# Kernel tuning notes

Measured on AMD Instinct MI355X. Metric: run time of the kernel, lower is better.

The kernel has to match this reference:

```python
import jax, jax.numpy as jnp
import numpy as np
import math

N, S, T, E, H = 2, 2048, 2048, 1024, 16
HD = E // H  # head_dim = 64


def setup_inputs() -> dict:
    key = jax.random.key(0)
    ks = jax.random.split(key, 11)
    scale = 1.0 / math.sqrt(E)
    inp = {
        "query": jax.random.normal(ks[0], (N, S, E), jnp.float32),
        "key": jax.random.normal(ks[1], (N, T, E), jnp.float32),
        "value": jax.random.normal(ks[2], (N, T, E), jnp.float32),
        "Wq": jax.random.normal(ks[3], (E, E), jnp.float32) * scale,
        "bq": jnp.zeros((E,), jnp.float32),
        "Wk": jax.random.normal(ks[4], (E, E), jnp.float32) * scale,
        "bk": jnp.zeros((E,), jnp.float32),
        "Wv": jax.random.normal(ks[5], (E, E), jnp.float32) * scale,
        "bv": jnp.zeros((E,), jnp.float32),
        "Wo": jax.random.normal(ks[6], (E, E), jnp.float32) * scale,
        "bo": jnp.zeros((E,), jnp.float32),
    }
    return inp


def reference(query, key, value, Wq, bq, Wk, bk, Wv, bv, Wo, bo):
    # QKV projections, then split heads: [N, S, E] -> [N, H, S, HD]
    q = (query @ Wq + bq).reshape(N, S, H, HD).transpose(0, 2, 1, 3)
    k = (key @ Wk + bk).reshape(N, T, H, HD).transpose(0, 2, 1, 3)
    v = (value @ Wv + bv).reshape(N, T, H, HD).transpose(0, 2, 1, 3)
    # scaled dot-product attention scores [N, H, S, T]
    scores = jnp.einsum('nhse,nhte->nhst', q, k) / math.sqrt(HD)
    attn = jax.nn.softmax(scores, axis=-1)
    # dropout is identity in eval mode
    out = jnp.einsum('nhst,nhte->nhse', attn, v)  # [N, H, S, HD]
    out = out.transpose(0, 2, 1, 3).reshape(N, S, E)
    return out @ Wo + bo
```

## Files before the change

### kernel.cpp

```cpp
#include <hip/hip_runtime.h>
#include <hip/hip_bf16.h>

typedef __bf16 bf16x8 __attribute__((ext_vector_type(8)));
typedef __bf16 bf16x4 __attribute__((ext_vector_type(4)));
typedef float  f32x4  __attribute__((ext_vector_type(4)));
typedef float  f32x16 __attribute__((ext_vector_type(16)));
typedef unsigned int u32x4 __attribute__((ext_vector_type(4)));

#define MFMA16(a, b, c) __builtin_amdgcn_mfma_f32_16x16x32_bf16((a), (b), (c), 0, 0, 0)
#define MFMA32(a, b, c) __builtin_amdgcn_mfma_f32_32x32x16_bf16((a), (b), (c), 0, 0, 0)

constexpr int SEQ = 2048, EMB = 1024, NHEAD = 16, HD = 64;
constexpr float SSCALE = 0.18033688f;

__device__ __forceinline__ void glds16(const void* g, void* l) {
    __builtin_amdgcn_global_load_lds(
        (const __attribute__((address_space(1))) void*)g,
        (__attribute__((address_space(3))) void*)l, 16, 0, 0);
}

__global__ __launch_bounds__(256)
void prep(const float* __restrict__ W0, const float* __restrict__ W1,
          const float* __restrict__ W2, const float* __restrict__ W3,
          __bf16* __restrict__ T0, __bf16* __restrict__ T1,
          __bf16* __restrict__ T2, __bf16* __restrict__ T3,
          const float* __restrict__ X0, const float* __restrict__ X1,
          const float* __restrict__ X2, __bf16* __restrict__ Y0,
          __bf16* __restrict__ Y1, __bf16* __restrict__ Y2)
{
    __shared__ float tile[32][33];
    const int z = blockIdx.z;
    if (z < 4) {
        const float* W = (z==0) ? W0 : (z==1) ? W1 : (z==2) ? W2 : W3;
        __bf16*      T = (z==0) ? T0 : (z==1) ? T1 : (z==2) ? T2 : T3;
        const float s = (z == 0) ? SSCALE : 1.0f;
        const int kb = blockIdx.x * 32, nb = blockIdx.y * 32;
        const int c = threadIdx.x & 31, r0 = threadIdx.x >> 5;
#pragma unroll
        for (int i = 0; i < 4; ++i)
            tile[r0 + 8*i][c] = W[(size_t)(kb + r0 + 8*i)*1024 + nb + c];
        __syncthreads();
#pragma unroll
        for (int i = 0; i < 4; ++i)
            T[(size_t)(nb + r0 + 8*i)*1024 + kb + c] = (__bf16)(tile[c][r0 + 8*i] * s);
    } else {
        const float* X = (z==4) ? X0 : (z==5) ? X1 : X2;
        __bf16*      Y = (z==4) ? Y0 : (z==5) ? Y1 : Y2;
        const size_t base =
            ((size_t)(blockIdx.y * 32 + blockIdx.x) * 256 + threadIdx.x) * 16;
#pragma unroll
        for (int j = 0; j < 2; ++j) {
            const float4* s4 = (const float4*)(X + base + j*8);
            float4 f0 = s4[0], f1 = s4[1];
            bf16x8 v;
            v[0]=(__bf16)f0.x; v[1]=(__bf16)f0.y; v[2]=(__bf16)f0.z; v[3]=(__bf16)f0.w;
            v[4]=(__bf16)f1.x; v[5]=(__bf16)f1.y; v[6]=(__bf16)f1.z; v[7]=(__bf16)f1.w;
            *(bf16x8*)(Y + base + j*8) = v;
        }
    }
}

struct GArg { const __bf16* A; const __bf16* Bt; const float* bias; void* C;
              int mode; int kbase; int kcount; float bscale; };
struct GArgs3 { GArg a[3]; };

__global__ __launch_bounds__(256)
void gemmk(GArgs3 args)
{
    const int lin = blockIdx.x + (blockIdx.y << 5) + (blockIdx.z << 8);
    const int nid = (lin & 7) * 96 + (lin >> 3);
    const int gz = nid >> 8, rem = nid & 255;
    const int bm = rem >> 3, bn = rem & 7;
    const GArg g = args.a[gz];
    __shared__ __attribute__((aligned(16))) __bf16 sm[2*128*64];
    __bf16* As = sm;
    __bf16* Bs = sm + 128*64;
    const int tid = threadIdx.x, lane = tid & 63, wave = tid >> 6;
    const int wm = wave >> 1, wn = wave & 1;
    const int quad = lane >> 4, l16 = lane & 15;

    f32x4 acc[4][4] = {};

    for (int kt = 0; kt < g.kcount; ++kt) {
        const int k0 = g.kbase + kt*64;
        __syncthreads();
#pragma unroll
        for (int j = 0; j < 4; ++j) {
            const int ci = j*256 + tid;
            const int row = ci >> 3, cg = ((ci & 7) ^ (row & 7)) * 8;
            glds16(g.A + (size_t)(bm*128 + row)*1024 + k0 + cg,
                   &As[(j*256 + wave*64)*8]);
        }
#pragma unroll
        for (int j = 0; j < 4; ++j) {
            const int ci = j*256 + tid;
            const int row = ci >> 3, cg = ((ci & 7) ^ (row & 7)) * 8;
            glds16(g.Bt + (size_t)(bn*128 + row)*1024 + k0 + cg,
                   &Bs[(j*256 + wave*64)*8]);
        }
        __syncthreads();
#pragma unroll
        for (int ks = 0; ks < 2; ++ks) {
            const int kc = ks*4 + quad;
            bf16x8 af[4], bfr[4];
#pragma unroll
            for (int mt = 0; mt < 4; ++mt) {
                const int ar = wm*64 + mt*16 + l16;
                af[mt] = *(const bf16x8*)&As[ar*64 + (kc ^ (ar & 7))*8];
            }
#pragma unroll
            for (int nt = 0; nt < 4; ++nt) {
                const int br = wn*64 + nt*16 + l16;
                bfr[nt] = *(const bf16x8*)&Bs[br*64 + (kc ^ (br & 7))*8];
            }
#pragma unroll
            for (int mt = 0; mt < 4; ++mt)
#pragma unroll
                for (int nt = 0; nt < 4; ++nt)
                    acc[mt][nt] = MFMA16(af[mt], bfr[nt], acc[mt][nt]);
        }
    }

    if (g.mode == 0) {
        __syncthreads();
        __bf16* Cs = sm;
#pragma unroll
        for (int nt = 0; nt < 4; ++nt) {
            const int n = wn*64 + nt*16 + l16;
            const float bvs = g.bias[bn*128 + n] * g.bscale;
#pragma unroll
            for (int mt = 0; mt < 4; ++mt) {
                const int mb = wm*64 + mt*16 + quad*4;
                f32x4 v = acc[mt][nt];
#pragma unroll
                for (int r = 0; r < 4; ++r) {
                    const int m = mb + r;
                    Cs[m*128 + (((n >> 3) ^ (m & 7)) * 8) + (n & 7)] =
                        (__bf16)(v[r] + bvs);
                }
            }
        }
        __syncthreads();
        __bf16* C = (__bf16*)g.C;
        const int p8 = tid & 7;
#pragma unroll
        for (int ps = 0; ps < 8; ++ps) {
            const int run = ps * 32 + (tid >> 3);
            const int m = run >> 1, hh = run & 1;
            const int gm = bm*128 + m;
            const int nb = gm >> 11, s = gm & 2047;
            const int h = bn*2 + hh;
            bf16x8 val = *(const bf16x8*)&Cs[m*128 + (((hh*8 + p8) ^ (m & 7)) * 8)];
            *(bf16x8*)&C[(size_t)(nb*NHEAD + h)*(SEQ*HD) + (size_t)s*HD + p8*8] = val;
        }
    } else {
#pragma unroll
        for (int nt = 0; nt < 4; ++nt) {
            const int n = bn*128 + wn*64 + nt*16 + l16;
            const float bvs = (g.bias ? g.bias[n] : 0.f) * g.bscale;
#pragma unroll
            for (int mt = 0; mt < 4; ++mt) {
                const int mbase = bm*128 + wm*64 + mt*16 + quad*4;
                f32x4 v = acc[mt][nt];
                __bf16* C = (__bf16*)g.C;
                const int h = n >> 6, d = n & 63;
                const int nb = mbase >> 11, s = mbase & 2047;
                const int tg = (s >> 2) & 7;
                const int pg = (tg & 4) | ((tg & 1) << 1) | ((tg & 2) >> 1);
                const int sp = (s & ~31) | (pg << 2);
                bf16x4 o;
#pragma unroll
                for (int r = 0; r < 4; ++r) o[r] = (__bf16)(v[r] + bvs);
                *(bf16x4*)&C[(size_t)(nb*NHEAD + h)*(SEQ*HD) + (size_t)d*SEQ + sp] = o;
            }
        }
    }
}

__global__ __launch_bounds__(256)
void gemmo(const __bf16* __restrict__ A, const __bf16* __restrict__ Bt,
           const float* __restrict__ bias, float* __restrict__ C)
{
    const int lin = blockIdx.x + (blockIdx.y << 5);
    const int nid = (lin & 7) * 32 + (lin >> 3);
    const int bm = nid >> 3, bn = nid & 7;
    __shared__ __attribute__((aligned(16))) __bf16 As[128*64];
    __shared__ __attribute__((aligned(16))) __bf16 Bs[128*64];
    const int tid = threadIdx.x, lane = tid & 63, wave = tid >> 6;
    const int wm = wave >> 1, wn = wave & 1;
    const int quad = lane >> 4, l16 = lane & 15;

    f32x4 acc[4][4] = {};

    for (int k0 = 0; k0 < 1024; k0 += 64) {
        __syncthreads();
#pragma unroll
        for (int j = 0; j < 4; ++j) {
            const int ci = j*256 + tid;
            const int row = ci >> 3, cg = ((ci & 7) ^ (row & 7)) * 8;
            glds16(A + (size_t)(bm*128 + row)*1024 + k0 + cg,
                   &As[(j*256 + wave*64)*8]);
        }
#pragma unroll
        for (int j = 0; j < 4; ++j) {
            const int ci = j*256 + tid;
            const int row = ci >> 3, cg = ((ci & 7) ^ (row & 7)) * 8;
            glds16(Bt + (size_t)(bn*128 + row)*1024 + k0 + cg,
                   &Bs[(j*256 + wave*64)*8]);
        }
        __syncthreads();
#pragma unroll
        for (int ks = 0; ks < 2; ++ks) {
            const int kc = ks*4 + quad;
            bf16x8 af[4], bfr[4];
#pragma unroll
            for (int mt = 0; mt < 4; ++mt) {
                const int ar = wm*64 + mt*16 + l16;
                af[mt] = *(const bf16x8*)&As[ar*64 + (kc ^ (ar & 7))*8];
            }
#pragma unroll
            for (int nt = 0; nt < 4; ++nt) {
                const int br = wn*64 + nt*16 + l16;
                bfr[nt] = *(const bf16x8*)&Bs[br*64 + (kc ^ (br & 7))*8];
            }
#pragma unroll
            for (int mt = 0; mt < 4; ++mt)
#pragma unroll
                for (int nt = 0; nt < 4; ++nt)
                    acc[mt][nt] = MFMA16(af[mt], bfr[nt], acc[mt][nt]);
        }
    }
#pragma unroll
    for (int nt = 0; nt < 4; ++nt) {
        const int n = bn*128 + wn*64 + nt*16 + l16;
        const float bv = bias[n];
#pragma unroll
        for (int mt = 0; mt < 4; ++mt) {
            const int mbase = bm*128 + wm*64 + mt*16 + quad*4;
            f32x4 v = acc[mt][nt];
#pragma unroll
            for (int r = 0; r < 4; ++r)
                C[(size_t)(mbase + r)*1024 + n] = v[r] + bv;
        }
    }
}

__global__ __launch_bounds__(512, 2)
void attn32(const __bf16* __restrict__ qg, const __bf16* __restrict__ kg,
            const __bf16* __restrict__ vg, __bf16* __restrict__ Og)
{
    __shared__ __attribute__((aligned(16))) char smem[64*1024];
    float* Xch = (float*)smem;

    const int tid = threadIdx.x, lane = tid & 63, wave = tid >> 6;
    const int w4 = wave & 3, grp = wave >> 2;
    const int l32 = lane & 31, half = lane >> 5;
    const int nh = blockIdx.y;
    const int q0 = blockIdx.x * 128;
    const __bf16* qb = qg + (size_t)nh * (SEQ*HD);
    const __bf16* kb = kg + (size_t)nh * (SEQ*HD);
    const __bf16* vb = vg + (size_t)nh * (SEQ*HD);

    bf16x8 qf[4];
#pragma unroll
    for (int ks = 0; ks < 4; ++ks)
        qf[ks] = *(const bf16x8*)(qb + (size_t)(q0 + w4*32 + l32)*HD + ks*16 + half*8);

    f32x16 oacc[2] = {};
    float psum = 0.0f;

    const int cK0 = tid, rK0 = cK0 >> 3;
    const int cK1 = 512 + tid, rK1 = cK1 >> 3;
    const __bf16* kp0 = kb + (size_t)rK0*HD + ((cK0 & 7) ^ (rK0 & 7)) * 8;
    const __bf16* kp1 = kb + (size_t)rK1*HD + ((cK1 & 7) ^ (rK1 & 7)) * 8;
    const int cV0 = tid, rV0 = cV0 >> 4, pV0 = cV0 & 15;
    const int cV1 = 512 + tid, rV1 = cV1 >> 4, pV1 = cV1 & 15;
    const __bf16* vp0 = vb + (size_t)rV0*SEQ + (((pV0 & ~7) | ((pV0 & 7) ^ (rV0 & 7))) * 8);
    const __bf16* vp1 = vb + (size_t)rV1*SEQ + (((pV1 & ~7) | ((pV1 & 7) ^ (rV1 & 7))) * 8);

    auto stage = [&](int b) {
        char* Kd = smem + b * 16384;
        char* Vd = smem + 32768 + b * 16384;
        glds16(kp0, Kd + wave*1024);
        glds16(kp1, Kd + 8192 + wave*1024);
        glds16(vp0, Vd + wave*1024);
        glds16(vp1, Vd + 8192 + wave*1024);
        kp0 += 128*HD; kp1 += 128*HD;
        vp0 += 128;    vp1 += 128;
    };

    stage(0);
    int cur = 0;
    for (int it = 0; it < 16; ++it) {
        __syncthreads();
        if (it < 15) stage(cur ^ 1);

        const __bf16* Ks = (const __bf16*)(smem + cur * 16384);
        const __bf16* Vs = (const __bf16*)(smem + 32768 + cur * 16384);

        f32x16 sc[2] = {};
        __builtin_amdgcn_s_setprio(1);
#pragma unroll
        for (int ks = 0; ks < 4; ++ks) {
            const int c = ks*2 + half;
#pragma unroll
            for (int nt = 0; nt < 2; ++nt) {
                const int kr = grp*64 + nt*32 + l32;
                bf16x8 kf = *(const bf16x8*)&Ks[kr*64 + ((c ^ (kr & 7))*8)];
                sc[nt] = MFMA32(kf, qf[ks], sc[nt]);
            }
        }
        __builtin_amdgcn_s_setprio(0);

#pragma unroll
        for (int nt = 0; nt < 2; ++nt)
#pragma unroll
            for (int sub = 0; sub < 2; ++sub) {
                const float e0 = __builtin_amdgcn_exp2f(sc[nt][sub*8 + 0]);
                const float e1 = __builtin_amdgcn_exp2f(sc[nt][sub*8 + 1]);
                const float e2 = __builtin_amdgcn_exp2f(sc[nt][sub*8 + 2]);
                const float e3 = __builtin_amdgcn_exp2f(sc[nt][sub*8 + 3]);
                const float e4 = __builtin_amdgcn_exp2f(sc[nt][sub*8 + 4]);
                const float e5 = __builtin_amdgcn_exp2f(sc[nt][sub*8 + 5]);
                const float e6 = __builtin_amdgcn_exp2f(sc[nt][sub*8 + 6]);
                const float e7 = __builtin_amdgcn_exp2f(sc[nt][sub*8 + 7]);
                psum += ((e0 + e1) + (e2 + e3)) + ((e4 + e5) + (e6 + e7));
                u32x4 pk;
                asm("v_cvt_pk_bf16_f32 %0, %1, %2" : "=v"(pk.x) : "v"(e0), "v"(e1));
                asm("v_cvt_pk_bf16_f32 %0, %1, %2" : "=v"(pk.y) : "v"(e2), "v"(e3));
                asm("v_cvt_pk_bf16_f32 %0, %1, %2" : "=v"(pk.z) : "v"(e4), "v"(e5));
                asm("v_cvt_pk_bf16_f32 %0, %1, %2" : "=v"(pk.w) : "v"(e6), "v"(e7));
                const bf16x8 pf = __builtin_bit_cast(bf16x8, pk);
                const int c2 = grp*8 + (nt*2 + sub)*2 + half;
                __builtin_amdgcn_s_setprio(1);
#pragma unroll
                for (int dt = 0; dt < 2; ++dt) {
                    const int vr = dt*32 + l32;
                    const int pos = (c2 & ~7) | ((c2 & 7) ^ (vr & 7));
                    bf16x8 vf = *(const bf16x8*)&Vs[vr*128 + pos*8];
                    oacc[dt] = MFMA32(pf, vf, oacc[dt]);
                }
                __builtin_amdgcn_s_setprio(0);
            }
        cur ^= 1;
    }

    __syncthreads();
    if (grp == 1) {
        float* dst = &Xch[((w4*64) + lane) * 33];
#pragma unroll
        for (int i = 0; i < 16; ++i) {
            dst[i]      = oacc[0][i];
            dst[16 + i] = oacc[1][i];
        }
        dst[32] = psum;
    }
    __syncthreads();
    if (grp == 0) {
        const float* src = &Xch[((w4*64) + lane) * 33];
#pragma unroll
        for (int i = 0; i < 16; ++i) {
            oacc[0][i] += src[i];
            oacc[1][i] += src[16 + i];
        }
        psum += src[32];
        psum += __shfl(psum, lane ^ 32);
        float* dl = (float*)(smem + 60*1024);
        if (half == 0) dl[w4*32 + l32] = psum;
        const int nb = nh >> 4, h = nh & 15;
#pragma unroll
        for (int reg = 0; reg < 16; ++reg) {
            const int row = (reg & 3) + 8*(reg >> 2) + 4*half;
            const int srow = q0 + w4*32 + row;
            const float inv = 1.0f / dl[w4*32 + row];
#pragma unroll
            for (int dt = 0; dt < 2; ++dt)
                Og[(size_t)(nb*SEQ + srow)*EMB + h*HD + dt*32 + l32] =
                    (__bf16)(oacc[dt][reg] * inv);
        }
    }
}

extern "C" void kernel_launch(void* const* d_in, const int* in_sizes, int n_in,
                              void* d_out, int out_size, void* d_ws, size_t ws_size,
                              hipStream_t stream)
{
    const float* query = (const float*)d_in[0];
    const float* key_  = (const float*)d_in[1];
    const float* value = (const float*)d_in[2];
    const float* Wq = (const float*)d_in[3];
    const float* bq = (const float*)d_in[4];
    const float* Wk = (const float*)d_in[5];
    const float* bk = (const float*)d_in[6];
    const float* Wv = (const float*)d_in[7];
    const float* bv = (const float*)d_in[8];
    const float* Wo = (const float*)d_in[9];
    const float* bo = (const float*)d_in[10];
    float* out = (float*)d_out;

    constexpr size_t SZW = 1024u*1024u;
    constexpr size_t SZX = 4096u*1024u;
    __bf16* ws  = (__bf16*)d_ws;
    __bf16* WqT = ws;
    __bf16* WkT = WqT + SZW;
    __bf16* WvT = WkT + SZW;
    __bf16* WoT = WvT + SZW;
    __bf16* xv  = WoT + SZW;
    __bf16* qh  = xv + SZX;
    __bf16* kh  = qh + SZX;
    __bf16* vTh = kh + SZX;
    __bf16* xq  = (__bf16*)d_out;
    __bf16* xk  = xq + SZX;
    __bf16* Oh  = xv;

    prep<<<dim3(32, 32, 7), 256, 0, stream>>>(Wq, Wk, Wv, Wo, WqT, WkT, WvT, WoT,
                                              query, key_, value, xq, xk, xv);
    GArgs3 a;
    a.a[0] = { xq, WqT, bq, qh,  0, 0, 16, SSCALE };
    a.a[1] = { xk, WkT, bk, kh,  0, 0, 16, 1.0f };
    a.a[2] = { xv, WvT, bv, vTh, 1, 0, 16, 1.0f };
    gemmk<<<dim3(32, 8, 3), 256, 0, stream>>>(a);
    attn32<<<dim3(16, 32), 512, 0, stream>>>(qh, kh, vTh, Oh);
    gemmo<<<dim3(32, 8), 256, 0, stream>>>(Oh, WoT, bo, out);
}
```

Measured before the change: 230.6 us.

## Double-buffer LDS tiles in projection and output GEMMs

Both GEMM kernels now use two LDS buffers. The next K-tile's global-to-LDS loads are issued right after the barrier, before the MFMA work on the current tile, and source pointers are precomputed and advanced incrementally. The goal is to hide global load latency behind compute and drop one barrier per iteration. In exchange, LDS per block doubles to 64KB, which can reduce occupancy. The overlap also depends on the compiler not waiting on every outstanding vmem load before the LDS reads.

After: 209.8 us (median of 3 runs). 1.1x faster.

```diff
diff --git a/kernel.cpp b/kernel.cpp
--- a/kernel.cpp
+++ b/kernel.cpp
@@ -72,33 +72,41 @@
     const int gz = nid >> 8, rem = nid & 255;
     const int bm = rem >> 3, bn = rem & 7;
     const GArg g = args.a[gz];
-    __shared__ __attribute__((aligned(16))) __bf16 sm[2*128*64];
-    __bf16* As = sm;
-    __bf16* Bs = sm + 128*64;
+    __shared__ __attribute__((aligned(16))) __bf16 sm[4*128*64];
     const int tid = threadIdx.x, lane = tid & 63, wave = tid >> 6;
     const int wm = wave >> 1, wn = wave & 1;
     const int quad = lane >> 4, l16 = lane & 15;
 
+    const __bf16* ap[4];
+    const __bf16* bp[4];
+#pragma unroll
+    for (int j = 0; j < 4; ++j) {
+        const int ci = j*256 + tid;
+        const int row = ci >> 3, cg = ((ci & 7) ^ (row & 7)) * 8;
+        ap[j] = g.A  + (size_t)(bm*128 + row)*1024 + g.kbase + cg;
+        bp[j] = g.Bt + (size_t)(bn*128 + row)*1024 + g.kbase + cg;
+    }
+
+    auto stage = [&](int b) {
+        __bf16* Ad = sm + b * 16384;
+        __bf16* Bd = Ad + 8192;
+#pragma unroll
+        for (int j = 0; j < 4; ++j) {
+            glds16(ap[j], &Ad[(j*256 + wave*64)*8]);
+            glds16(bp[j], &Bd[(j*256 + wave*64)*8]);
+            ap[j] += 64; bp[j] += 64;
+        }
+    };
+
     f32x4 acc[4][4] = {};
 
+    stage(0);
+    int cur = 0;
     for (int kt = 0; kt < g.kcount; ++kt) {
-        const int k0 = g.kbase + kt*64;
-        __syncthreads();
-#pragma unroll
-        for (int j = 0; j < 4; ++j) {
-            const int ci = j*256 + tid;
-            const int row = ci >> 3, cg = ((ci & 7) ^ (row & 7)) * 8;
-            glds16(g.A + (size_t)(bm*128 + row)*1024 + k0 + cg,
-                   &As[(j*256 + wave*64)*8]);
-        }
-#pragma unroll
-        for (int j = 0; j < 4; ++j) {
-            const int ci = j*256 + tid;
-            const int row = ci >> 3, cg = ((ci & 7) ^ (row & 7)) * 8;
-            glds16(g.Bt + (size_t)(bn*128 + row)*1024 + k0 + cg,
-                   &Bs[(j*256 + wave*64)*8]);
-        }
-        __syncthreads();
+        __syncthreads();
+        if (kt < g.kcount - 1) stage(cur ^ 1);
+        const __bf16* As = sm + cur * 16384;
+        const __bf16* Bs = As + 8192;
 #pragma unroll
         for (int ks = 0; ks < 2; ++ks) {
             const int kc = ks*4 + quad;
@@ -119,6 +127,7 @@
                 for (int nt = 0; nt < 4; ++nt)
                     acc[mt][nt] = MFMA16(af[mt], bfr[nt], acc[mt][nt]);
         }
+        cur ^= 1;
     }
 
     if (g.mode == 0) {
@@ -184,31 +193,41 @@
     const int lin = blockIdx.x + (blockIdx.y << 5);
     const int nid = (lin & 7) * 32 + (lin >> 3);
     const int bm = nid >> 3, bn = nid & 7;
-    __shared__ __attribute__((aligned(16))) __bf16 As[128*64];
-    __shared__ __attribute__((aligned(16))) __bf16 Bs[128*64];
+    __shared__ __attribute__((aligned(16))) __bf16 sm[4*128*64];
     const int tid = threadIdx.x, lane = tid & 63, wave = tid >> 6;
     const int wm = wave >> 1, wn = wave & 1;
     const int quad = lane >> 4, l16 = lane & 15;
 
+    const __bf16* ap[4];
+    const __bf16* bp[4];
+#pragma unroll
+    for (int j = 0; j < 4; ++j) {
+        const int ci = j*256 + tid;
+        const int row = ci >> 3, cg = ((ci & 7) ^ (row & 7)) * 8;
+        ap[j] = A  + (size_t)(bm*128 + row)*1024 + cg;
+        bp[j] = Bt + (size_t)(bn*128 + row)*1024 + cg;
+    }
+
+    auto stage = [&](int b) {
+        __bf16* Ad = sm + b * 16384;
+        __bf16* Bd = Ad + 8192;
+#pragma unroll
+        for (int j = 0; j < 4; ++j) {
+            glds16(ap[j], &Ad[(j*256 + wave*64)*8]);
+            glds16(bp[j], &Bd[(j*256 + wave*64)*8]);
+            ap[j] += 64; bp[j] += 64;
+        }
+    };
+
     f32x4 acc[4][4] = {};
 
-    for (int k0 = 0; k0 < 1024; k0 += 64) {
-        __syncthreads();
-#pragma unroll
-        for (int j = 0; j < 4; ++j) {
-            const int ci = j*256 + tid;
-            const int row = ci >> 3, cg = ((ci & 7) ^ (row & 7)) * 8;
-            glds16(A + (size_t)(bm*128 + row)*1024 + k0 + cg,
-                   &As[(j*256 + wave*64)*8]);
-        }
-#pragma unroll
-        for (int j = 0; j < 4; ++j) {
-            const int ci = j*256 + tid;
-            const int row = ci >> 3, cg = ((ci & 7) ^ (row & 7)) * 8;
-            glds16(Bt + (size_t)(bn*128 + row)*1024 + k0 + cg,
-                   &Bs[(j*256 + wave*64)*8]);
-        }
-        __syncthreads();
+    stage(0);
+    int cur = 0;
+    for (int kt = 0; kt < 16; ++kt) {
+        __syncthreads();
+        if (kt < 15) stage(cur ^ 1);
+        const __bf16* As = sm + cur * 16384;
+        const __bf16* Bs = As + 8192;
 #pragma unroll
         for (int ks = 0; ks < 2; ++ks) {
             const int kc = ks*4 + quad;
@@ -229,6 +248,7 @@
                 for (int nt = 0; nt < 4; ++nt)
                     acc[mt][nt] = MFMA16(af[mt], bfr[nt], acc[mt][nt]);
         }
+        cur ^= 1;
     }
 #pragma unroll
     for (int nt = 0; nt < 4; ++nt) {
```
